# Kernel tuning notes

Hardware: AMD Instinct MI355X
Metric: run time of the kernel (lower is better)

Reference implementation:

```python
import jax, jax.numpy as jnp
import numpy as np

N_NODES = 20000
N_EDGES = 320000
IN_F = 256
HID = 64
OUT_F = 64
EDGE_F = 16
HEADS = 4
NUM_CLASSES = 10
NUM_GRAPHS = 40
ALPHA = 0.2  # LeakyReLU negative slope


def _xavier(key, shape):
    fan_in, fan_out = shape[0], shape[-1]
    std = 1.414 * np.sqrt(2.0 / (fan_in + fan_out))
    return jax.random.normal(key, shape, dtype=jnp.float32) * std


def setup_inputs() -> dict:
    key = jax.random.key(0)
    ks = jax.random.split(key, 12)
    x = jax.random.normal(ks[0], (N_NODES, IN_F), dtype=jnp.float32)
    edge_index = jax.random.randint(ks[1], (2, N_EDGES), 0, N_NODES, dtype=jnp.int32)
    edge_attr = jax.random.uniform(ks[2], (N_EDGES, EDGE_F), dtype=jnp.float32)
    batch = jnp.sort(jax.random.randint(ks[3], (N_NODES,), 0, NUM_GRAPHS, dtype=jnp.int32))
    # layer 0: in=IN_F, heads=HEADS, out=HID, concat
    W0 = _xavier(ks[4], (IN_F, HEADS * HID))
    a0 = _xavier(ks[5], (HEADS, 2 * HID + EDGE_F))
    # layer 1: in=HID*HEADS, heads=HEADS, out=HID, concat
    W1 = _xavier(ks[6], (HID * HEADS, HEADS * HID))
    a1 = _xavier(ks[7], (HEADS, 2 * HID + EDGE_F))
    # layer 2: in=HID*HEADS, heads=1, out=OUT_F, mean over heads
    W2 = _xavier(ks[8], (HID * HEADS, 1 * OUT_F))
    a2 = _xavier(ks[9], (1, 2 * OUT_F + EDGE_F))
    cls_w = _xavier(ks[10], (OUT_F, NUM_CLASSES))
    cls_b = jnp.zeros((NUM_CLASSES,), dtype=jnp.float32)
    return {"x": x, "edge_index": edge_index, "edge_attr": edge_attr, "batch": batch,
            "W0": W0, "a0": a0, "W1": W1, "a1": a1, "W2": W2, "a2": a2,
            "cls_w": cls_w, "cls_b": cls_b}


def gat_layer(h, W, a, edge_index, edge_attr, heads, out_f, concat):
    n = h.shape[0]
    Wh = (h @ W).reshape(n, heads, out_f)              # [N,H,D]
    src, dst = edge_index[0], edge_index[1]
    a_i, a_j, a_e = a[:, :out_f], a[:, out_f:2 * out_f], a[:, 2 * out_f:]
    # per-node head scores, gathered per edge (equivalent to concat + dot with a)
    s_i = jnp.einsum('nhd,hd->nh', Wh, a_i)            # [N,H]
    s_j = jnp.einsum('nhd,hd->nh', Wh, a_j)            # [N,H]
    s_e = edge_attr @ a_e.T                            # [E,H]
    e = s_i[src] + s_j[dst] + s_e                      # [E,H]
    e = jnp.where(e > 0, e, ALPHA * e)                 # LeakyReLU
    # NB: faithful to source — softmax over the HEADS dim (dim=1), not per-node
    att = jax.nn.softmax(e, axis=1)                    # [E,H]
    msg = att[:, :, None] * Wh[dst]                    # [E,H,D]
    h_prime = jax.ops.segment_sum(msg, src, num_segments=n)  # scatter-add to src
    if concat:
        return jax.nn.elu(h_prime.reshape(n, heads * out_f))
    return h_prime.mean(axis=1)


def reference(x, edge_index, edge_attr, batch, W0, a0, W1, a1, W2, a2, cls_w, cls_b):
    h = gat_layer(x, W0, a0, edge_index, edge_attr, HEADS, HID, True)
    h = gat_layer(h, W1, a1, edge_index, edge_attr, HEADS, HID, True)
    h = gat_layer(h, W2, a2, edge_index, edge_attr, 1, OUT_F, False)
    # global mean pool over graphs
    sums = jax.ops.segment_sum(h, batch, num_segments=NUM_GRAPHS)
    cnts = jax.ops.segment_sum(jnp.ones((h.shape[0],), h.dtype), batch, num_segments=NUM_GRAPHS)
    pooled = sums / jnp.maximum(cnts, 1.0)[:, None]
    logits = pooled @ cls_w + cls_b
    return jax.nn.log_softmax(logits, axis=1)
```

## Files before the change

kernel.cpp:

```cpp
#include <hip/hip_runtime.h>
#include <hip/hip_bf16.h>
#include <math.h>

#define N_NODES 20000
#define N_EDGES 320000
#define IN_F 256
#define HID 64
#define HEADS 4
#define OUT_F 64
#define EDGE_F 16
#define NUM_CLASSES 10
#define NUM_GRAPHS 40
#define LRELU_ALPHA 0.2f

typedef short bf16x8 __attribute__((ext_vector_type(8)));
typedef unsigned short u16x8 __attribute__((ext_vector_type(8)));
typedef float f32x4 __attribute__((ext_vector_type(4)));

static __device__ __forceinline__ float bf2f(unsigned short u) {
    union { unsigned int i; float f; } v; v.i = ((unsigned int)u) << 16; return v.f;
}
static __device__ __forceinline__ unsigned short f2bf(float f) {
    union { float f; unsigned int i; } v; v.f = f;
    unsigned int r = v.i + 0x7FFF + ((v.i >> 16) & 1);
    return (unsigned short)(r >> 16);
}
static __device__ __forceinline__ float eluf(float a) {
    return a > 0.f ? a : __expf(a) - 1.0f;
}

__global__ void f2bf_kernel(const float* __restrict__ in, unsigned short* __restrict__ out, int n4) {
    int i = blockIdx.x * blockDim.x + threadIdx.x;
    if (i >= n4) return;
    float4 v = ((const float4*)in)[i];
    ushort4 o;
    o.x = f2bf(v.x); o.y = f2bf(v.y); o.z = f2bf(v.z); o.w = f2bf(v.w);
    ((ushort4*)out)[i] = o;
}

__global__ void count_kernel(const int* __restrict__ src, int* __restrict__ cnt) {
    int e = blockIdx.x * blockDim.x + threadIdx.x;
    if (e < N_EDGES) atomicAdd(&cnt[src[e]], 1);
}

__global__ __launch_bounds__(1024) void scan_kernel(const int* __restrict__ cnt,
                                                    int* __restrict__ row_ptr) {
    __shared__ int wsum[16];
    __shared__ int carry_s;
    int t = threadIdx.x;
    int lane = t & 63, wave = t >> 6;
    if (t == 0) { carry_s = 0; row_ptr[0] = 0; }
    __syncthreads();
    for (int base = 0; base < N_NODES; base += 1024) {
        int idx = base + t;
        int x = (idx < N_NODES) ? cnt[idx] : 0;
#pragma unroll
        for (int off = 1; off < 64; off <<= 1) {
            int y = __shfl_up(x, off, 64);
            if (lane >= off) x += y;
        }
        if (lane == 63) wsum[wave] = x;
        __syncthreads();
        if (wave == 0 && lane < 16) {
            int s = wsum[lane];
#pragma unroll
            for (int off = 1; off < 16; off <<= 1) {
                int y = __shfl_up(s, off, 64);
                if (lane >= off) s += y;
            }
            wsum[lane] = s;
        }
        __syncthreads();
        int waveoff = (wave > 0) ? wsum[wave - 1] : 0;
        int carry = carry_s;
        if (idx < N_NODES) row_ptr[idx + 1] = x + waveoff + carry;
        __syncthreads();
        if (t == 0) carry_s = carry + wsum[15];
        __syncthreads();
    }
}

__global__ void scatter_kernel(const int* __restrict__ src, const int* __restrict__ dst,
                               const float* __restrict__ ea, const int* __restrict__ row_ptr,
                               int* __restrict__ cursor, int* __restrict__ srcp,
                               int* __restrict__ dstp, float* __restrict__ eap) {
    int e = blockIdx.x * blockDim.x + threadIdx.x;
    if (e < N_EDGES) {
        int s = src[e];
        int pos = row_ptr[s] + atomicAdd(&cursor[s], 1);
        srcp[pos] = s;
        dstp[pos] = dst[e];
#pragma unroll
        for (int k = 0; k < 4; ++k)
            ((float4*)(eap + (size_t)pos * 16))[k] = ((const float4*)(ea + (size_t)e * 16))[k];
    }
}

template <bool AF32>
__global__ __launch_bounds__(256) void gemm_bf16(const void* __restrict__ Aptr,
                                                 const unsigned short* __restrict__ B,
                                                 unsigned short* __restrict__ C,
                                                 int M, int N, int K) {
    __shared__ unsigned short As[64][40];
    __shared__ unsigned short Bs[64][40];
    __shared__ unsigned short Cs[64][72];
    int tid = threadIdx.x;
    int bm = blockIdx.x * 64, bn = blockIdx.y * 64;
    int w = tid >> 6, l = tid & 63;
    int wr = (w >> 1) * 32, wc = (w & 1) * 32;
    int lr = l & 15, lk = (l >> 4) * 8;
    f32x4 acc[2][2] = {};
    int ar = tid >> 2, akc = (tid & 3) * 8;
    int bk = tid >> 3, bn8 = tid & 7, bnc = bn8 * 8;

    for (int k0 = 0; k0 < K; k0 += 32) {
        bf16x8 av = {};
        if (bm + ar < M) {
            if constexpr (AF32) {
                const float* Af = (const float*)Aptr + (size_t)(bm + ar) * K + k0 + akc;
                float4 f0 = *(const float4*)Af;
                float4 f1 = *(const float4*)(Af + 4);
                av[0] = (short)f2bf(f0.x); av[1] = (short)f2bf(f0.y);
                av[2] = (short)f2bf(f0.z); av[3] = (short)f2bf(f0.w);
                av[4] = (short)f2bf(f1.x); av[5] = (short)f2bf(f1.y);
                av[6] = (short)f2bf(f1.z); av[7] = (short)f2bf(f1.w);
            } else {
                av = *(const bf16x8*)((const unsigned short*)Aptr + (size_t)(bm + ar) * K + k0 + akc);
            }
        }
        *(bf16x8*)&As[ar][akc] = av;
        bf16x8 bv = *(const bf16x8*)(B + (size_t)(k0 + bk) * N + bn + bnc);
#pragma unroll
        for (int j = 0; j < 8; ++j) {
            int jj = (j + bn8) & 7;
            Bs[bnc + jj][bk] = (unsigned short)bv[jj];
        }
        __syncthreads();
        bf16x8 a0 = *(const bf16x8*)&As[wr + lr][lk];
        bf16x8 a1 = *(const bf16x8*)&As[wr + 16 + lr][lk];
        bf16x8 b0 = *(const bf16x8*)&Bs[wc + lr][lk];
        bf16x8 b1 = *(const bf16x8*)&Bs[wc + 16 + lr][lk];
        acc[0][0] = __builtin_amdgcn_mfma_f32_16x16x32_bf16(a0, b0, acc[0][0], 0, 0, 0);
        acc[0][1] = __builtin_amdgcn_mfma_f32_16x16x32_bf16(a0, b1, acc[0][1], 0, 0, 0);
        acc[1][0] = __builtin_amdgcn_mfma_f32_16x16x32_bf16(a1, b0, acc[1][0], 0, 0, 0);
        acc[1][1] = __builtin_amdgcn_mfma_f32_16x16x32_bf16(a1, b1, acc[1][1], 0, 0, 0);
        __syncthreads();
    }
#pragma unroll
    for (int i = 0; i < 2; ++i)
#pragma unroll
        for (int j = 0; j < 2; ++j)
#pragma unroll
            for (int r = 0; r < 4; ++r)
                Cs[wr + i * 16 + (l >> 4) * 4 + r][wc + j * 16 + (l & 15)] = f2bf(acc[i][j][r]);
    __syncthreads();
    int row = tid >> 3, cc = (tid & 7) * 8;
#pragma unroll
    for (int p = 0; p < 2; ++p, row += 32) {
        if (bm + row < M) {
            bf16x8 o = *(const bf16x8*)&Cs[row][cc];
            *(bf16x8*)(C + (size_t)(bm + row) * N + bn + cc) = o;
        }
    }
}

__global__ void node_scores(const unsigned short* __restrict__ Wh, const float* __restrict__ a,
                            float* __restrict__ si, float* __restrict__ sj) {
    __shared__ float sa[HEADS * 144];
    int tid = threadIdx.x;
    for (int i = tid; i < HEADS * 144; i += blockDim.x) sa[i] = a[i];
    __syncthreads();
    int gid = blockIdx.x * blockDim.x + tid;
    if (gid >= N_NODES * HEADS) return;
    int h = gid & 3;
    const unsigned short* w = Wh + (size_t)(gid >> 2) * 256 + h * 64;
    const float* ai = sa + h * 144;
    const float* aj = ai + 64;
    float s0 = 0.f, s1 = 0.f;
#pragma unroll
    for (int d = 0; d < 64; d += 8) {
        bf16x8 wv = *(const bf16x8*)(w + d);
#pragma unroll
        for (int j = 0; j < 8; ++j) {
            float f = bf2f((unsigned short)wv[j]);
            s0 += f * ai[d + j];
            s1 += f * aj[d + j];
        }
    }
    si[gid] = s0;
    sj[gid] = s1;
}

__global__ void att_kernel(const int* __restrict__ srcp, const int* __restrict__ dstp,
                           const float* __restrict__ eap, const float* __restrict__ a,
                           const float* __restrict__ si, const float* __restrict__ sj,
                           float* __restrict__ attp) {
    __shared__ float ae[HEADS][EDGE_F];
    int tid = threadIdx.x;
    if (tid < HEADS * EDGE_F) ae[tid >> 4][tid & 15] = a[(tid >> 4) * 144 + 128 + (tid & 15)];
    __syncthreads();
    int i = blockIdx.x * blockDim.x + tid;
    if (i >= N_EDGES) return;
    int s = srcp[i], u = dstp[i];
    float4 siv = ((const float4*)si)[s];
    float4 sjv = ((const float4*)sj)[u];
    float x[16];
#pragma unroll
    for (int k = 0; k < 16; k += 4) {
        float4 v = *(const float4*)(eap + (size_t)i * 16 + k);
        x[k] = v.x; x[k + 1] = v.y; x[k + 2] = v.z; x[k + 3] = v.w;
    }
    float se0 = 0.f, se1 = 0.f, se2 = 0.f, se3 = 0.f;
#pragma unroll
    for (int k = 0; k < 16; ++k) {
        se0 += x[k] * ae[0][k];
        se1 += x[k] * ae[1][k];
        se2 += x[k] * ae[2][k];
        se3 += x[k] * ae[3][k];
    }
    float t0 = siv.x + sjv.x + se0;
    float t1 = siv.y + sjv.y + se1;
    float t2 = siv.z + sjv.z + se2;
    float t3 = siv.w + sjv.w + se3;
    t0 = t0 > 0.f ? t0 : LRELU_ALPHA * t0;
    t1 = t1 > 0.f ? t1 : LRELU_ALPHA * t1;
    t2 = t2 > 0.f ? t2 : LRELU_ALPHA * t2;
    t3 = t3 > 0.f ? t3 : LRELU_ALPHA * t3;
    float m = fmaxf(fmaxf(t0, t1), fmaxf(t2, t3));
    float p0 = __expf(t0 - m), p1 = __expf(t1 - m), p2 = __expf(t2 - m), p3 = __expf(t3 - m);
    float inv = 1.0f / (p0 + p1 + p2 + p3);
    ((float4*)attp)[i] = make_float4(p0 * inv, p1 * inv, p2 * inv, p3 * inv);
}

__global__ __launch_bounds__(256) void edge_agg_concat(
    const unsigned short* __restrict__ Whb, const float* __restrict__ attp,
    const int* __restrict__ row_ptr, const int* __restrict__ dstp,
    unsigned short* __restrict__ out) {
    int v = blockIdx.x * 4 + (threadIdx.x >> 6);
    if (v >= N_NODES) return;
    int l = threadIdx.x & 63;
    int half = l >> 5, p = l & 31;
    int h = p >> 3;
    int beg = row_ptr[v], end = row_ptr[v + 1];
    float acc[8] = {};
    int i = beg + half;
    int u_n = 0; float at_n = 0.f;
    if (i < end) { u_n = dstp[i]; at_n = attp[(size_t)i * 4 + h]; }
    for (; i < end; i += 2) {
        int u = u_n;
        float at = at_n;
        if (i + 2 < end) { u_n = dstp[i + 2]; at_n = attp[(size_t)(i + 2) * 4 + h]; }
        u16x8 wv = *(const u16x8*)(Whb + (size_t)u * 256 + p * 8);
#pragma unroll
        for (int j = 0; j < 8; ++j) acc[j] += at * bf2f(wv[j]);
    }
#pragma unroll
    for (int j = 0; j < 8; ++j) acc[j] += __shfl_xor(acc[j], 32, 64);
    if (half == 0) {
        u16x8 o;
#pragma unroll
        for (int j = 0; j < 8; ++j) o[j] = f2bf(eluf(acc[j]));
        *(u16x8*)(out + (size_t)v * 256 + p * 8) = o;
    }
}

__global__ __launch_bounds__(256) void edge_agg_single(
    const unsigned short* __restrict__ Whb, const int* __restrict__ row_ptr,
    const int* __restrict__ dstp, float* __restrict__ out) {
    int v = blockIdx.x * 4 + (threadIdx.x >> 6);
    if (v >= N_NODES) return;
    int l = threadIdx.x & 63;
    int q = l >> 4, p = l & 15;
    int beg = row_ptr[v], end = row_ptr[v + 1];
    float acc[4] = {};
    for (int i = beg + q; i < end; i += 4) {
        int u = dstp[i];
        ushort4 w = *(const ushort4*)(Whb + (size_t)u * 64 + p * 4);
        acc[0] += bf2f(w.x); acc[1] += bf2f(w.y); acc[2] += bf2f(w.z); acc[3] += bf2f(w.w);
    }
#pragma unroll
    for (int j = 0; j < 4; ++j) {
        acc[j] += __shfl_xor(acc[j], 16, 64);
        acc[j] += __shfl_xor(acc[j], 32, 64);
    }
    if (l < 16) {
        float4 o = make_float4(acc[0], acc[1], acc[2], acc[3]);
        *(float4*)(out + (size_t)v * 64 + p * 4) = o;
    }
}

__global__ __launch_bounds__(1024) void pool_kernel(const float* __restrict__ h3,
                                                    const int* __restrict__ batch,
                                                    float* __restrict__ pooled) {
    int g = blockIdx.x;
    int lane = threadIdx.x & 63;
    int wave = threadIdx.x >> 6;
    int lo = 0, hi = N_NODES;
    while (lo < hi) { int mid = (lo + hi) >> 1; if (batch[mid] < g) lo = mid + 1; else hi = mid; }
    int start = lo;
    lo = start; hi = N_NODES;
    while (lo < hi) { int mid = (lo + hi) >> 1; if (batch[mid] < g + 1) lo = mid + 1; else hi = mid; }
    int endi = lo;
    float s = 0.f;
    for (int v = start + wave; v < endi; v += 16) s += h3[(size_t)v * 64 + lane];
    __shared__ float red[16][64];
    red[wave][lane] = s;
    __syncthreads();
    if (wave == 0) {
        float t = red[0][lane];
#pragma unroll
        for (int w = 1; w < 16; ++w) t += red[w][lane];
        float c = (float)((endi - start) > 1 ? (endi - start) : 1);
        pooled[g * 64 + lane] = t / c;
    }
}

__global__ void classify_kernel(const float* __restrict__ pooled, const float* __restrict__ cw,
                                const float* __restrict__ cb, float* __restrict__ out) {
    int g = threadIdx.x;
    if (g >= NUM_GRAPHS) return;
    float lg[NUM_CLASSES];
#pragma unroll
    for (int c = 0; c < NUM_CLASSES; ++c) lg[c] = cb[c];
    for (int d = 0; d < OUT_F; ++d) {
        float p = pooled[g * 64 + d];
#pragma unroll
        for (int c = 0; c < NUM_CLASSES; ++c) lg[c] += p * cw[d * NUM_CLASSES + c];
    }
    float m = lg[0];
#pragma unroll
    for (int c = 1; c < NUM_CLASSES; ++c) m = fmaxf(m, lg[c]);
    float s = 0.f;
#pragma unroll
    for (int c = 0; c < NUM_CLASSES; ++c) s += expf(lg[c] - m);
    float lse = m + logf(s);
#pragma unroll
    for (int c = 0; c < NUM_CLASSES; ++c) out[g * NUM_CLASSES + c] = lg[c] - lse;
}

extern "C" void kernel_launch(void* const* d_in, const int* in_sizes, int n_in,
                              void* d_out, int out_size, void* d_ws, size_t ws_size,
                              hipStream_t stream) {
    const float* x   = (const float*)d_in[0];
    const int*   ei  = (const int*)d_in[1];
    const float* ea  = (const float*)d_in[2];
    const int* batch = (const int*)d_in[3];
    const float* W0  = (const float*)d_in[4];
    const float* a0  = (const float*)d_in[5];
    const float* W1  = (const float*)d_in[6];
    const float* a1  = (const float*)d_in[7];
    const float* W2  = (const float*)d_in[8];
    const float* cw  = (const float*)d_in[10];
    const float* cb  = (const float*)d_in[11];
    float* out = (float*)d_out;

    const int* srcg = ei;
    const int* dstg = ei + N_EDGES;

    char* ws = (char*)d_ws;
    size_t off = 0;
    auto alloc = [&](size_t bytes) -> char* {
        char* p = ws + off;
        off += (bytes + 255) & ~(size_t)255;
        return p;
    };
    unsigned short* W0b  = (unsigned short*)alloc(256 * 256 * 2);
    unsigned short* W1b  = (unsigned short*)alloc(256 * 256 * 2);
    unsigned short* W2b  = (unsigned short*)alloc(256 * 64 * 2);
    unsigned short* Whb  = (unsigned short*)alloc((size_t)N_NODES * 256 * 2);
    unsigned short* hAb  = (unsigned short*)alloc((size_t)N_NODES * 256 * 2);
    unsigned short* hBb  = (unsigned short*)alloc((size_t)N_NODES * 256 * 2);
    unsigned short* Wh2b = (unsigned short*)alloc((size_t)N_NODES * 64 * 2);
    float* si   = (float*)alloc((size_t)N_NODES * HEADS * 4);
    float* sj   = (float*)alloc((size_t)N_NODES * HEADS * 4);
    float* attp = (float*)alloc((size_t)N_EDGES * HEADS * 4);
    float* eap  = (float*)alloc((size_t)N_EDGES * EDGE_F * 4);
    int* row_ptr = (int*)alloc((N_NODES + 1) * 4);
    int* cnt  = (int*)alloc(N_NODES * 4);
    int* srcp = (int*)alloc(N_EDGES * 4);
    int* dstp = (int*)alloc(N_EDGES * 4);
    float* h3 = (float*)alloc((size_t)N_NODES * 64 * 4);
    float* pooled = (float*)alloc(NUM_GRAPHS * 64 * 4);

    f2bf_kernel<<<(256 * 256 / 4 + 255) / 256, 256, 0, stream>>>(W0, W0b, 256 * 256 / 4);
    f2bf_kernel<<<(256 * 256 / 4 + 255) / 256, 256, 0, stream>>>(W1, W1b, 256 * 256 / 4);
    f2bf_kernel<<<(256 * 64 / 4 + 255) / 256, 256, 0, stream>>>(W2, W2b, 256 * 64 / 4);

    hipMemsetAsync(cnt, 0, N_NODES * 4, stream);
    count_kernel<<<(N_EDGES + 255) / 256, 256, 0, stream>>>(srcg, cnt);
    scan_kernel<<<1, 1024, 0, stream>>>(cnt, row_ptr);
    hipMemsetAsync(cnt, 0, N_NODES * 4, stream);
    scatter_kernel<<<(N_EDGES + 255) / 256, 256, 0, stream>>>(srcg, dstg, ea, row_ptr, cnt,
                                                              srcp, dstp, eap);

    dim3 ggrid((N_NODES + 63) / 64, 4);
    dim3 ggrid2((N_NODES + 63) / 64, 1);
    int nsb = (N_NODES * HEADS + 255) / 256;
    int atb = (N_EDGES + 255) / 256;
    int agb = (N_NODES + 3) / 4;

    gemm_bf16<true><<<ggrid, 256, 0, stream>>>(x, W0b, Whb, N_NODES, 256, 256);
    node_scores<<<nsb, 256, 0, stream>>>(Whb, a0, si, sj);
    att_kernel<<<atb, 256, 0, stream>>>(srcp, dstp, eap, a0, si, sj, attp);
    edge_agg_concat<<<agb, 256, 0, stream>>>(Whb, attp, row_ptr, dstp, hAb);

    gemm_bf16<false><<<ggrid, 256, 0, stream>>>(hAb, W1b, Whb, N_NODES, 256, 256);
    node_scores<<<nsb, 256, 0, stream>>>(Whb, a1, si, sj);
    att_kernel<<<atb, 256, 0, stream>>>(srcp, dstp, eap, a1, si, sj, attp);
    edge_agg_concat<<<agb, 256, 0, stream>>>(Whb, attp, row_ptr, dstp, hBb);

    gemm_bf16<false><<<ggrid2, 256, 0, stream>>>(hBb, W2b, Wh2b, N_NODES, 64, 256);
    edge_agg_single<<<agb, 256, 0, stream>>>(Wh2b, row_ptr, dstp, h3);

    pool_kernel<<<NUM_GRAPHS, 1024, 0, stream>>>(h3, batch, pooled);
    classify_kernel<<<1, 64, 0, stream>>>(pooled, cw, cb, out);
}
```

Before: 225.8 us.

## Fuse node scores into GEMM, merge weight conversions, widen edge aggregation loops

Node attention scores are now computed in the GEMM epilogue from the shared-memory C tile, so the separate node_scores kernel and its re-read of Wh are gone. The three weight-conversion launches become one kernel. The scan writes scatter cursors directly, which removes a memset and a row_ptr read in scatter. The edge aggregation kernels process four or eight edges per wave iteration with 16-byte loads and float4 attention reads, adding shuffle reductions, to expose more memory parallelism. This costs extra shuffles and registers, and the sa load in the GEMM relies on later barriers in the K loop before it is read.

```diff
diff --git a/kernel.cpp b/kernel.cpp
--- a/kernel.cpp
+++ b/kernel.cpp
@@ -29,13 +29,19 @@
     return a > 0.f ? a : __expf(a) - 1.0f;
 }
 
-__global__ void f2bf_kernel(const float* __restrict__ in, unsigned short* __restrict__ out, int n4) {
+__global__ void wconv_kernel(const float* __restrict__ W0, const float* __restrict__ W1,
+                             const float* __restrict__ W2, unsigned short* __restrict__ W0b,
+                             unsigned short* __restrict__ W1b, unsigned short* __restrict__ W2b) {
     int i = blockIdx.x * blockDim.x + threadIdx.x;
-    if (i >= n4) return;
-    float4 v = ((const float4*)in)[i];
+    const float* src; unsigned short* dst; int off;
+    if (i < 16384)      { src = W0; dst = W0b; off = i; }
+    else if (i < 32768) { src = W1; dst = W1b; off = i - 16384; }
+    else if (i < 36864) { src = W2; dst = W2b; off = i - 32768; }
+    else return;
+    float4 v = ((const float4*)src)[off];
     ushort4 o;
     o.x = f2bf(v.x); o.y = f2bf(v.y); o.z = f2bf(v.z); o.w = f2bf(v.w);
-    ((ushort4*)out)[i] = o;
+    ((ushort4*)dst)[off] = o;
 }
 
 __global__ void count_kernel(const int* __restrict__ src, int* __restrict__ cnt) {
@@ -44,7 +50,8 @@
 }
 
 __global__ __launch_bounds__(1024) void scan_kernel(const int* __restrict__ cnt,
-                                                    int* __restrict__ row_ptr) {
+                                                    int* __restrict__ row_ptr,
+                                                    int* __restrict__ cursor) {
     __shared__ int wsum[16];
     __shared__ int carry_s;
     int t = threadIdx.x;
@@ -53,7 +60,8 @@
     __syncthreads();
     for (int base = 0; base < N_NODES; base += 1024) {
         int idx = base + t;
-        int x = (idx < N_NODES) ? cnt[idx] : 0;
+        int x0 = (idx < N_NODES) ? cnt[idx] : 0;
+        int x = x0;
 #pragma unroll
         for (int off = 1; off < 64; off <<= 1) {
             int y = __shfl_up(x, off, 64);
@@ -73,7 +81,11 @@
         __syncthreads();
         int waveoff = (wave > 0) ? wsum[wave - 1] : 0;
         int carry = carry_s;
-        if (idx < N_NODES) row_ptr[idx + 1] = x + waveoff + carry;
+        if (idx < N_NODES) {
+            int incl = x + waveoff + carry;
+            row_ptr[idx + 1] = incl;
+            cursor[idx] = incl - x0;
+        }
         __syncthreads();
         if (t == 0) carry_s = carry + wsum[15];
         __syncthreads();
@@ -81,13 +93,13 @@
 }
 
 __global__ void scatter_kernel(const int* __restrict__ src, const int* __restrict__ dst,
-                               const float* __restrict__ ea, const int* __restrict__ row_ptr,
-                               int* __restrict__ cursor, int* __restrict__ srcp,
-                               int* __restrict__ dstp, float* __restrict__ eap) {
+                               const float* __restrict__ ea, int* __restrict__ cursor,
+                               int* __restrict__ srcp, int* __restrict__ dstp,
+                               float* __restrict__ eap) {
     int e = blockIdx.x * blockDim.x + threadIdx.x;
     if (e < N_EDGES) {
         int s = src[e];
-        int pos = row_ptr[s] + atomicAdd(&cursor[s], 1);
+        int pos = atomicAdd(&cursor[s], 1);
         srcp[pos] = s;
         dstp[pos] = dst[e];
 #pragma unroll
@@ -96,15 +108,19 @@
     }
 }
 
-template <bool AF32>
+template <bool AF32, bool SCORES>
 __global__ __launch_bounds__(256) void gemm_bf16(const void* __restrict__ Aptr,
                                                  const unsigned short* __restrict__ B,
                                                  unsigned short* __restrict__ C,
+                                                 const float* __restrict__ avec,
+                                                 float* __restrict__ si, float* __restrict__ sj,
                                                  int M, int N, int K) {
     __shared__ unsigned short As[64][40];
     __shared__ unsigned short Bs[64][40];
     __shared__ unsigned short Cs[64][72];
+    __shared__ float sa[128];
     int tid = threadIdx.x;
+    if (SCORES && tid < 128) sa[tid] = avec[blockIdx.y * 144 + tid];
     int bm = blockIdx.x * 64, bn = blockIdx.y * 64;
     int w = tid >> 6, l = tid & 63;
     int wr = (w >> 1) * 32, wc = (w & 1) * 32;
@@ -162,33 +178,22 @@
             *(bf16x8*)(C + (size_t)(bm + row) * N + bn + cc) = o;
         }
     }
-}
-
-__global__ void node_scores(const unsigned short* __restrict__ Wh, const float* __restrict__ a,
-                            float* __restrict__ si, float* __restrict__ sj) {
-    __shared__ float sa[HEADS * 144];
-    int tid = threadIdx.x;
-    for (int i = tid; i < HEADS * 144; i += blockDim.x) sa[i] = a[i];
-    __syncthreads();
-    int gid = blockIdx.x * blockDim.x + tid;
-    if (gid >= N_NODES * HEADS) return;
-    int h = gid & 3;
-    const unsigned short* w = Wh + (size_t)(gid >> 2) * 256 + h * 64;
-    const float* ai = sa + h * 144;
-    const float* aj = ai + 64;
-    float s0 = 0.f, s1 = 0.f;
-#pragma unroll
-    for (int d = 0; d < 64; d += 8) {
-        bf16x8 wv = *(const bf16x8*)(w + d);
-#pragma unroll
-        for (int j = 0; j < 8; ++j) {
-            float f = bf2f((unsigned short)wv[j]);
-            s0 += f * ai[d + j];
-            s1 += f * aj[d + j];
-        }
-    }
-    si[gid] = s0;
-    sj[gid] = s1;
+    if (SCORES) {
+        int r = tid >> 2, qq = tid & 3;
+        float s0 = 0.f, s1 = 0.f;
+#pragma unroll
+        for (int k = 0; k < 16; ++k) {
+            float f = bf2f(Cs[r][qq * 16 + k]);
+            s0 += f * sa[qq * 16 + k];
+            s1 += f * sa[64 + qq * 16 + k];
+        }
+        s0 += __shfl_xor(s0, 1, 64); s0 += __shfl_xor(s0, 2, 64);
+        s1 += __shfl_xor(s1, 1, 64); s1 += __shfl_xor(s1, 2, 64);
+        if (qq == 0 && bm + r < M) {
+            si[(size_t)(bm + r) * 4 + blockIdx.y] = s0;
+            sj[(size_t)(bm + r) * 4 + blockIdx.y] = s1;
+        }
+    }
 }
 
 __global__ void att_kernel(const int* __restrict__ srcp, const int* __restrict__ dstp,
@@ -239,28 +244,43 @@
     int v = blockIdx.x * 4 + (threadIdx.x >> 6);
     if (v >= N_NODES) return;
     int l = threadIdx.x & 63;
-    int half = l >> 5, p = l & 31;
-    int h = p >> 3;
+    int slot = l >> 4, p = l & 15;
     int beg = row_ptr[v], end = row_ptr[v + 1];
-    float acc[8] = {};
-    int i = beg + half;
-    int u_n = 0; float at_n = 0.f;
-    if (i < end) { u_n = dstp[i]; at_n = attp[(size_t)i * 4 + h]; }
-    for (; i < end; i += 2) {
+    float acc0[8] = {}, acc1[8] = {};
+    int i = beg + slot;
+    int u_n = 0;
+    float4 at_n = make_float4(0.f, 0.f, 0.f, 0.f);
+    if (i < end) { u_n = dstp[i]; at_n = ((const float4*)attp)[i]; }
+    for (; i < end; i += 4) {
         int u = u_n;
-        float at = at_n;
-        if (i + 2 < end) { u_n = dstp[i + 2]; at_n = attp[(size_t)(i + 2) * 4 + h]; }
-        u16x8 wv = *(const u16x8*)(Whb + (size_t)u * 256 + p * 8);
-#pragma unroll
-        for (int j = 0; j < 8; ++j) acc[j] += at * bf2f(wv[j]);
-    }
-#pragma unroll
-    for (int j = 0; j < 8; ++j) acc[j] += __shfl_xor(acc[j], 32, 64);
-    if (half == 0) {
-        u16x8 o;
-#pragma unroll
-        for (int j = 0; j < 8; ++j) o[j] = f2bf(eluf(acc[j]));
-        *(u16x8*)(out + (size_t)v * 256 + p * 8) = o;
+        float4 at4 = at_n;
+        if (i + 4 < end) { u_n = dstp[i + 4]; at_n = ((const float4*)attp)[i + 4]; }
+        const unsigned short* row = Whb + (size_t)u * 256;
+        u16x8 w0 = *(const u16x8*)(row + p * 8);
+        u16x8 w1 = *(const u16x8*)(row + 128 + p * 8);
+        float atA = (p & 8) ? at4.y : at4.x;
+        float atB = (p & 8) ? at4.w : at4.z;
+#pragma unroll
+        for (int j = 0; j < 8; ++j) acc0[j] += atA * bf2f(w0[j]);
+#pragma unroll
+        for (int j = 0; j < 8; ++j) acc1[j] += atB * bf2f(w1[j]);
+    }
+#pragma unroll
+    for (int j = 0; j < 8; ++j) {
+        acc0[j] += __shfl_xor(acc0[j], 16, 64);
+        acc0[j] += __shfl_xor(acc0[j], 32, 64);
+        acc1[j] += __shfl_xor(acc1[j], 16, 64);
+        acc1[j] += __shfl_xor(acc1[j], 32, 64);
+    }
+    if (slot == 0) {
+        u16x8 o0, o1;
+#pragma unroll
+        for (int j = 0; j < 8; ++j) {
+            o0[j] = f2bf(eluf(acc0[j]));
+            o1[j] = f2bf(eluf(acc1[j]));
+        }
+        *(u16x8*)(out + (size_t)v * 256 + p * 8) = o0;
+        *(u16x8*)(out + (size_t)v * 256 + 128 + p * 8) = o1;
     }
 }
 
@@ -270,22 +290,30 @@
     int v = blockIdx.x * 4 + (threadIdx.x >> 6);
     if (v >= N_NODES) return;
     int l = threadIdx.x & 63;
-    int q = l >> 4, p = l & 15;
+    int slot = l >> 3, p = l & 7;
     int beg = row_ptr[v], end = row_ptr[v + 1];
-    float acc[4] = {};
-    for (int i = beg + q; i < end; i += 4) {
-        int u = dstp[i];
-        ushort4 w = *(const ushort4*)(Whb + (size_t)u * 64 + p * 4);
-        acc[0] += bf2f(w.x); acc[1] += bf2f(w.y); acc[2] += bf2f(w.z); acc[3] += bf2f(w.w);
-    }
-#pragma unroll
-    for (int j = 0; j < 4; ++j) {
+    float acc[8] = {};
+    int i = beg + slot;
+    int u_n = 0;
+    if (i < end) u_n = dstp[i];
+    for (; i < end; i += 8) {
+        int u = u_n;
+        if (i + 8 < end) u_n = dstp[i + 8];
+        u16x8 w = *(const u16x8*)(Whb + (size_t)u * 64 + p * 8);
+#pragma unroll
+        for (int j = 0; j < 8; ++j) acc[j] += bf2f(w[j]);
+    }
+#pragma unroll
+    for (int j = 0; j < 8; ++j) {
+        acc[j] += __shfl_xor(acc[j], 8, 64);
         acc[j] += __shfl_xor(acc[j], 16, 64);
         acc[j] += __shfl_xor(acc[j], 32, 64);
     }
-    if (l < 16) {
-        float4 o = make_float4(acc[0], acc[1], acc[2], acc[3]);
-        *(float4*)(out + (size_t)v * 64 + p * 4) = o;
+    if (l < 8) {
+        float4 o0 = make_float4(acc[0], acc[1], acc[2], acc[3]);
+        float4 o1 = make_float4(acc[4], acc[5], acc[6], acc[7]);
+        *(float4*)(out + (size_t)v * 64 + p * 8) = o0;
+        *(float4*)(out + (size_t)v * 64 + p * 8 + 4) = o1;
     }
 }
 
@@ -376,40 +404,36 @@
     float* attp = (float*)alloc((size_t)N_EDGES * HEADS * 4);
     float* eap  = (float*)alloc((size_t)N_EDGES * EDGE_F * 4);
     int* row_ptr = (int*)alloc((N_NODES + 1) * 4);
+    int* cursor  = (int*)alloc(N_NODES * 4);
     int* cnt  = (int*)alloc(N_NODES * 4);
     int* srcp = (int*)alloc(N_EDGES * 4);
     int* dstp = (int*)alloc(N_EDGES * 4);
     float* h3 = (float*)alloc((size_t)N_NODES * 64 * 4);
     float* pooled = (float*)alloc(NUM_GRAPHS * 64 * 4);
 
-    f2bf_kernel<<<(256 * 256 / 4 + 255) / 256, 256, 0, stream>>>(W0, W0b, 256 * 256 / 4);
-    f2bf_kernel<<<(256 * 256 / 4 + 255) / 256, 256, 0, stream>>>(W1, W1b, 256 * 256 / 4);
-    f2bf_kernel<<<(256 * 64 / 4 + 255) / 256, 256, 0, stream>>>(W2, W2b, 256 * 64 / 4);
+    wconv_kernel<<<144, 256, 0, stream>>>(W0, W1, W2, W0b, W1b, W2b);
 
     hipMemsetAsync(cnt, 0, N_NODES * 4, stream);
     count_kernel<<<(N_EDGES + 255) / 256, 256, 0, stream>>>(srcg, cnt);
-    scan_kernel<<<1, 1024, 0, stream>>>(cnt, row_ptr);
-    hipMemsetAsync(cnt, 0, N_NODES * 4, stream);
-    scatter_kernel<<<(N_EDGES + 255) / 256, 256, 0, stream>>>(srcg, dstg, ea, row_ptr, cnt,
+    scan_kernel<<<1, 1024, 0, stream>>>(cnt, row_ptr, cursor);
+    scatter_kernel<<<(N_EDGES + 255) / 256, 256, 0, stream>>>(srcg, dstg, ea, cursor,
                                                               srcp, dstp, eap);
 
     dim3 ggrid((N_NODES + 63) / 64, 4);
     dim3 ggrid2((N_NODES + 63) / 64, 1);
-    int nsb = (N_NODES * HEADS + 255) / 256;
     int atb = (N_EDGES + 255) / 256;
     int agb = (N_NODES + 3) / 4;
 
-    gemm_bf16<true><<<ggrid, 256, 0, stream>>>(x, W0b, Whb, N_NODES, 256, 256);
-    node_scores<<<nsb, 256, 0, stream>>>(Whb, a0, si, sj);
+    gemm_bf16<true, true><<<ggrid, 256, 0, stream>>>(x, W0b, Whb, a0, si, sj, N_NODES, 256, 256);
     att_kernel<<<atb, 256, 0, stream>>>(srcp, dstp, eap, a0, si, sj, attp);
     edge_agg_concat<<<agb, 256, 0, stream>>>(Whb, attp, row_ptr, dstp, hAb);
 
-    gemm_bf16<false><<<ggrid, 256, 0, stream>>>(hAb, W1b, Whb, N_NODES, 256, 256);
-    node_scores<<<nsb, 256, 0, stream>>>(Whb, a1, si, sj);
+    gemm_bf16<false, true><<<ggrid, 256, 0, stream>>>(hAb, W1b, Whb, a1, si, sj, N_NODES, 256, 256);
     att_kernel<<<atb, 256, 0, stream>>>(srcp, dstp, eap, a1, si, sj, attp);
     edge_agg_concat<<<agb, 256, 0, stream>>>(Whb, attp, row_ptr, dstp, hBb);
 
-    gemm_bf16<false><<<ggrid2, 256, 0, stream>>>(hBb, W2b, Wh2b, N_NODES, 64, 256);
+    gemm_bf16<false, false><<<ggrid2, 256, 0, stream>>>(hBb, W2b, Wh2b, nullptr, nullptr, nullptr,
+                                                        N_NODES, 64, 256);
     edge_agg_single<<<agb, 256, 0, stream>>>(Wh2b, row_ptr, dstp, h3);
 
     pool_kernel<<<NUM_GRAPHS, 1024, 0, stream>>>(h3, batch, pooled);
```

New measurement: 209.3 us. 7.3% less time.
